# Kernel optimization log

Hardware: AMD Instinct MI355X
Metric: run time of the kernel (lower is better)

## Reference

```python
import jax, jax.numpy as jnp
import numpy as np

TAU = 2.0
V_TH = 1.0
ALPHA = 2.0  # ATan surrogate alpha (spikingjelly default)

@jax.custom_vjp
def atan_heaviside(x):
    # Forward: Heaviside spike; backward: ATan surrogate gradient.
    return (x >= 0).astype(x.dtype)

def _atan_fwd(x):
    return atan_heaviside(x), x

def _atan_bwd(x, g):
    sg = (ALPHA / 2.0) / (1.0 + (jnp.pi / 2.0 * ALPHA * x) ** 2)
    return (g * sg,)

atan_heaviside.defvjp(_atan_fwd, _atan_bwd)

def lif_scan(cur):
    # cur: [T, B, F] input currents. LIF: H = V + (X - V)/tau; S = H >= v_th; hard reset V = H*(1-S).
    def step(v, x_t):
        h = v + (x_t - v) / TAU
        s = atan_heaviside(h - V_TH)
        v_new = h * (1.0 - s)
        return v_new, s
    v0 = jnp.zeros(cur.shape[1:], dtype=cur.dtype)
    _, spikes = jax.lax.scan(step, v0, cur)
    return spikes

def setup_inputs() -> dict:
    key = jax.random.key(0)
    k1, k2 = jax.random.split(key)
    T, B, F_in, F_out = 64, 256, 1024, 1024
    x = jax.random.normal(k1, (T, B, F_in), dtype=jnp.float32)
    W = jax.random.normal(k2, (F_out, F_in), dtype=jnp.float32) * (1.0 / np.sqrt(F_in))
    return {"x": x, "W": W}

def reference(x, W):
    # Linear projection over all timesteps, then multi-step LIF recurrence.
    cur = jnp.einsum('tbf,of->tbo', x, W)  # [T, B, F_out]
    return lif_scan(cur)
```

## Files before the change

### kernel.cpp

```cpp
#include <hip/hip_runtime.h>


#define T_DIM 64
#define B_DIM 256
#define F_DIM 1024
#define K_DIM 1024
#define M_DIM 16384
#define COLS  (B_DIM * F_DIM)
#define KP    2048
#define MARGIN 6e-5f
#define LIST_CAP 32768

typedef __attribute__((ext_vector_type(8))) short short8;
typedef __attribute__((ext_vector_type(4))) float floatx4;

#define ASYNC_CP16(gp, lp)                                                     \
    __builtin_amdgcn_global_load_lds(                                          \
        (const __attribute__((address_space(1))) unsigned int*)(gp),           \
        (__attribute__((address_space(3))) unsigned int*)(lp), 16, 0, 0)

__device__ inline unsigned short f32_to_bf16_rne(float f) {
    unsigned int u = __builtin_bit_cast(unsigned int, f);
    unsigned int r = (u + 0x7FFFu + ((u >> 16) & 1u)) >> 16;
    return (unsigned short)r;
}
__device__ inline float bf16_to_f32(unsigned short h) {
    unsigned int u = ((unsigned int)h) << 16;
    return __builtin_bit_cast(float, u);
}

__global__ __launch_bounds__(256) void split_kernel(
    const float* __restrict__ x, const float* __restrict__ Wm,
    unsigned short* __restrict__ A, unsigned short* __restrict__ B,
    unsigned int* __restrict__ counter)
{
    if (blockIdx.x == 0 && threadIdx.x == 0) *counter = 0;
    const int blk = blockIdx.x;
    const float* in;
    unsigned short* dst;
    int g;
    int orow;
    if (blk < 16384) {
        g = blk * 256 + threadIdx.x;
        int e = g * 4;
        int row = e >> 10;
        orow = ((row & 255) << 6) | (row >> 8);
        in = x; dst = A;
    } else {
        g = (blk - 16384) * 256 + threadIdx.x;
        int e = g * 4;
        orow = e >> 10;
        in = Wm; dst = B;
    }
    int k = (g * 4) & 1023;
    float4 v = reinterpret_cast<const float4*>(in)[g];
    ushort4 h, l;
    float f;
    f = v.x; h.x = f32_to_bf16_rne(f); l.x = f32_to_bf16_rne(f - bf16_to_f32(h.x));
    f = v.y; h.y = f32_to_bf16_rne(f); l.y = f32_to_bf16_rne(f - bf16_to_f32(h.y));
    f = v.z; h.z = f32_to_bf16_rne(f); l.z = f32_to_bf16_rne(f - bf16_to_f32(h.z));
    f = v.w; h.w = f32_to_bf16_rne(f); l.w = f32_to_bf16_rne(f - bf16_to_f32(h.w));
    reinterpret_cast<ushort4*>(dst)[(size_t)orow * (KP / 4) + (k >> 2)] = h;
    reinterpret_cast<ushort4*>(dst)[(size_t)orow * (KP / 4) + 256 + (k >> 2)] = l;
}

__global__ __launch_bounds__(256, 2) void gemm_scan_kernel(
    const unsigned short* __restrict__ A,
    const unsigned short* __restrict__ B,
    float* __restrict__ out,
    unsigned int* __restrict__ counter, unsigned int* __restrict__ list)
{
    __shared__ unsigned short Ah[128 * 32];
    __shared__ unsigned short Al[128 * 32];
    __shared__ unsigned short Bh[256 * 32];
    __shared__ unsigned short Bl[256 * 32];

    const int tid  = threadIdx.x;
    const int lane = tid & 63;
    const int wv   = tid >> 6;
    const int lid = blockIdx.x;
    const int mt  = ((lid & 7) << 4) | (lid >> 5);
    const int nt  = (lid >> 3) & 3;
    const int m0  = mt * 128;
    const int n0  = nt * 256;
    const int wm  = (wv & 1) * 64;
    const int wn  = (wv >> 1) * 128;

    floatx4 acc[4][8] = {};

    const int srow = tid >> 2;
    const int slin = (tid & 3) * 8;
    const int ssw  = (((tid & 3) ^ ((tid >> 3) & 3)) * 8);
    const int lrow = lane & 15;
    const int q    = lane >> 4;
    const int rsw  = (lrow >> 1) & 3;

    const unsigned short* Ab = A + (size_t)m0 * KP;
    const unsigned short* Bb = B + (size_t)n0 * KP;

    for (int k0 = 0; k0 < 1024; k0 += 32) {
        __syncthreads();
        ASYNC_CP16(Ab + (size_t)srow * KP + k0 + ssw,                Ah + srow * 32 + slin);
        ASYNC_CP16(Ab + (size_t)(srow + 64) * KP + k0 + ssw,         Ah + (srow + 64) * 32 + slin);
        ASYNC_CP16(Ab + (size_t)srow * KP + 1024 + k0 + ssw,         Al + srow * 32 + slin);
        ASYNC_CP16(Ab + (size_t)(srow + 64) * KP + 1024 + k0 + ssw,  Al + (srow + 64) * 32 + slin);
        ASYNC_CP16(Bb + (size_t)srow * KP + k0 + ssw,                Bh + srow * 32 + slin);
        ASYNC_CP16(Bb + (size_t)(srow + 64) * KP + k0 + ssw,         Bh + (srow + 64) * 32 + slin);
        ASYNC_CP16(Bb + (size_t)(srow + 128) * KP + k0 + ssw,        Bh + (srow + 128) * 32 + slin);
        ASYNC_CP16(Bb + (size_t)(srow + 192) * KP + k0 + ssw,        Bh + (srow + 192) * 32 + slin);
        ASYNC_CP16(Bb + (size_t)srow * KP + 1024 + k0 + ssw,         Bl + srow * 32 + slin);
        ASYNC_CP16(Bb + (size_t)(srow + 64) * KP + 1024 + k0 + ssw,  Bl + (srow + 64) * 32 + slin);
        ASYNC_CP16(Bb + (size_t)(srow + 128) * KP + 1024 + k0 + ssw, Bl + (srow + 128) * 32 + slin);
        ASYNC_CP16(Bb + (size_t)(srow + 192) * KP + 1024 + k0 + ssw, Bl + (srow + 192) * 32 + slin);
        __syncthreads();

        const int sl = (q ^ rsw) * 8;
        short8 ah[4], al[4];
#pragma unroll
        for (int i = 0; i < 4; ++i) {
            ah[i] = *reinterpret_cast<const short8*>(&Ah[(wm + i * 16 + lrow) * 32 + sl]);
            al[i] = *reinterpret_cast<const short8*>(&Al[(wm + i * 16 + lrow) * 32 + sl]);
        }
#pragma unroll
        for (int jh = 0; jh < 2; ++jh) {
            short8 bh[4], bl[4];
#pragma unroll
            for (int j4 = 0; j4 < 4; ++j4) {
                const int jr = (wn + (jh * 4 + j4) * 16 + lrow) * 32 + sl;
                bh[j4] = *reinterpret_cast<const short8*>(&Bh[jr]);
                bl[j4] = *reinterpret_cast<const short8*>(&Bl[jr]);
            }
#pragma unroll
            for (int i = 0; i < 4; ++i)
#pragma unroll
                for (int j4 = 0; j4 < 4; ++j4)
                    acc[i][jh * 4 + j4] = __builtin_amdgcn_mfma_f32_16x16x32_bf16(
                        ah[i], bh[j4], acc[i][jh * 4 + j4], 0, 0, 0);
#pragma unroll
            for (int i = 0; i < 4; ++i)
#pragma unroll
                for (int j4 = 0; j4 < 4; ++j4)
                    acc[i][jh * 4 + j4] = __builtin_amdgcn_mfma_f32_16x16x32_bf16(
                        al[i], bh[j4], acc[i][jh * 4 + j4], 0, 0, 0);
#pragma unroll
            for (int i = 0; i < 4; ++i)
#pragma unroll
                for (int j4 = 0; j4 < 4; ++j4)
                    acc[i][jh * 4 + j4] = __builtin_amdgcn_mfma_f32_16x16x32_bf16(
                        ah[i], bl[j4], acc[i][jh * 4 + j4], 0, 0, 0);
        }
    }

    const int col = lane & 15;
    const int b_g = mt * 2 + (wv & 1);

    unsigned int fmask = 0;
#pragma unroll
    for (int j = 0; j < 8; ++j) {
        float v = 0.f;
        bool fl = false;
#pragma unroll
        for (int i = 0; i < 4; ++i) {
#pragma unroll
            for (int qq = 0; qq < 4; ++qq) {
                if (q == qq) {
#pragma unroll
                    for (int r = 0; r < 4; ++r) {
                        float cu = acc[i][j][r];
                        float h = v + (cu - v) * 0.5f;
                        float d = h - 1.0f;
                        bool sp = (d >= 0.f);
                        fl |= (fabsf(d) < MARGIN);
                        acc[i][j][r] = sp ? 1.0f : 0.0f;
                        v = sp ? 0.f : h;
                    }
                }
                v = __shfl(v, qq * 16 + col, 64);
            }
        }
        if (fl) fmask |= (1u << j);
    }
    fmask |= __shfl_xor(fmask, 16, 64);
    fmask |= __shfl_xor(fmask, 32, 64);

    float* outp = out + (size_t)b_g * F_DIM;
#pragma unroll
    for (int i = 0; i < 4; ++i)
#pragma unroll
        for (int j = 0; j < 8; ++j)
#pragma unroll
            for (int r = 0; r < 4; ++r) {
                int t = i * 16 + q * 4 + r;
                int o = n0 + wn + j * 16 + col;
                outp[(size_t)t * COLS + o] = acc[i][j][r];
            }

    if (q == 0 && fmask) {
        for (int j = 0; j < 8; ++j)
            if (fmask & (1u << j)) {
                unsigned int idx = atomicAdd(counter, 1u);
                if (idx < LIST_CAP)
                    list[idx] = (unsigned int)((b_g << 10) | (n0 + wn + j * 16 + col));
            }
    }
}

__global__ __launch_bounds__(256) void fixup_kernel(
    const float* __restrict__ x, const float* __restrict__ W,
    const unsigned int* __restrict__ counter, const unsigned int* __restrict__ list,
    float* __restrict__ out)
{
    __shared__ double curd[T_DIM];
    __shared__ float wrow[K_DIM];
    unsigned int n = *counter;
    if (n > LIST_CAP) n = LIST_CAP;
    const int wv = threadIdx.x >> 6, lane = threadIdx.x & 63;

    for (unsigned int idx = blockIdx.x; idx < n; idx += gridDim.x) {
        const unsigned int c = list[idx];
        const int b = c >> 10, o = c & 1023;
        __syncthreads();
        for (int k = threadIdx.x; k < K_DIM; k += 256) wrow[k] = W[(size_t)o * K_DIM + k];
        __syncthreads();
        for (int it = 0; it < 16; ++it) {
            const int t = it * 4 + wv;
            const float* xp = x + (size_t)t * COLS + (size_t)b * F_DIM + lane * 16;
            double s = 0.0;
#pragma unroll
            for (int qq = 0; qq < 4; ++qq) {
                float4 xv = reinterpret_cast<const float4*>(xp)[qq];
                float4 wq = *reinterpret_cast<const float4*>(&wrow[lane * 16 + qq * 4]);
                s += (double)xv.x * (double)wq.x + (double)xv.y * (double)wq.y +
                     (double)xv.z * (double)wq.z + (double)xv.w * (double)wq.w;
            }
#pragma unroll
            for (int off = 32; off > 0; off >>= 1) s += __shfl_down(s, off, 64);
            if (lane == 0) curd[t] = s;
        }
        __syncthreads();
        if (threadIdx.x == 0) {
            double v = 0.0;
            for (int t = 0; t < T_DIM; ++t) {
                double h = v + (curd[t] - v) * 0.5;
                bool s = (h >= 1.0);
                out[(size_t)t * COLS + c] = s ? 1.0f : 0.0f;
                v = s ? 0.0 : h;
            }
        }
        __syncthreads();
    }
}

#define TILE 64
#define KC 32
#define XS_LD 36
#define SC_LD 65

__global__ __launch_bounds__(256) void lif_fused_kernel(
    const float* __restrict__ x, const float* __restrict__ Wm, float* __restrict__ out)
{
    __shared__ __align__(16) unsigned char smem_raw[TILE * SC_LD * sizeof(double)];
    float* sf = reinterpret_cast<float*>(smem_raw);
    double* sd = reinterpret_cast<double*>(smem_raw);
    float* Xs = sf;
    float* Ws = sf + TILE * XS_LD;

    const int b = blockIdx.y;
    const int o0 = blockIdx.x * TILE;
    const int tid = threadIdx.x;
    const int tx = tid & 15, ty = tid >> 4;

    double acc[4][4];
#pragma unroll
    for (int i = 0; i < 4; ++i)
#pragma unroll
        for (int j = 0; j < 4; ++j) acc[i][j] = 0.0;

    const int r = tid >> 3, c4 = (tid & 7) * 4;
    const float* xbase = x + (size_t)b * F_DIM;

    for (int k0 = 0; k0 < K_DIM; k0 += KC) {
        __syncthreads();
        float4 xv0 = *reinterpret_cast<const float4*>(xbase + (size_t)r * COLS + k0 + c4);
        float4 xv1 = *reinterpret_cast<const float4*>(xbase + (size_t)(r + 32) * COLS + k0 + c4);
        *reinterpret_cast<float4*>(Xs + r * XS_LD + c4) = xv0;
        *reinterpret_cast<float4*>(Xs + (r + 32) * XS_LD + c4) = xv1;
        float4 wv0 = *reinterpret_cast<const float4*>(Wm + (size_t)(o0 + r) * K_DIM + k0 + c4);
        float4 wv1 = *reinterpret_cast<const float4*>(Wm + (size_t)(o0 + r + 32) * K_DIM + k0 + c4);
        *reinterpret_cast<float4*>(Ws + r * XS_LD + c4) = wv0;
        *reinterpret_cast<float4*>(Ws + (r + 32) * XS_LD + c4) = wv1;
        __syncthreads();
#pragma unroll 4
        for (int kk = 0; kk < KC; ++kk) {
            double xa[4], wb[4];
#pragma unroll
            for (int i = 0; i < 4; ++i) xa[i] = (double)Xs[(4 * ty + i) * XS_LD + kk];
#pragma unroll
            for (int j = 0; j < 4; ++j) wb[j] = (double)Ws[(4 * tx + j) * XS_LD + kk];
#pragma unroll
            for (int i = 0; i < 4; ++i)
#pragma unroll
                for (int j = 0; j < 4; ++j) acc[i][j] = fma(xa[i], wb[j], acc[i][j]);
        }
    }
    __syncthreads();
#pragma unroll
    for (int i = 0; i < 4; ++i)
#pragma unroll
        for (int j = 0; j < 4; ++j) sd[(4 * ty + i) * SC_LD + (4 * tx + j)] = acc[i][j];
    __syncthreads();
    if (tid < TILE) {
        double v = 0.0;
        float* outp = out + (size_t)b * F_DIM + o0 + tid;
        for (int t = 0; t < T_DIM; ++t) {
            double cu = sd[t * SC_LD + tid];
            double h = v + (cu - v) * 0.5;
            bool s = (h >= 1.0);
            outp[(size_t)t * COLS] = s ? 1.0f : 0.0f;
            v = s ? 0.0 : h;
        }
    }
}

extern "C" void kernel_launch(void* const* d_in, const int* in_sizes, int n_in,
                              void* d_out, int out_size, void* d_ws, size_t ws_size,
                              hipStream_t stream) {
    const float* x = (const float*)d_in[0];
    const float* Wm = (const float*)d_in[1];
    float* out = (float*)d_out;

    const size_t OFF_A   = 0;
    const size_t OFF_B   = OFF_A + (size_t)M_DIM * KP * 2;
    const size_t OFF_CNT = OFF_B + (size_t)F_DIM * KP * 2;
    const size_t OFF_LST = OFF_CNT + 256;
    const size_t NEEDED  = OFF_LST + (size_t)LIST_CAP * 4;

    if (ws_size < NEEDED) {
        dim3 grid(F_DIM / TILE, B_DIM, 1);
        lif_fused_kernel<<<grid, dim3(256), 0, stream>>>(x, Wm, out);
        return;
    }

    unsigned char* ws = (unsigned char*)d_ws;
    unsigned short* Abuf = (unsigned short*)(ws + OFF_A);
    unsigned short* Bbuf = (unsigned short*)(ws + OFF_B);
    unsigned int* counter = (unsigned int*)(ws + OFF_CNT);
    unsigned int* list = (unsigned int*)(ws + OFF_LST);

    split_kernel<<<dim3(16384 + 1024), dim3(256), 0, stream>>>(x, Wm, Abuf, Bbuf, counter);
    gemm_scan_kernel<<<dim3(512), dim3(256), 0, stream>>>(Abuf, Bbuf, out, counter, list);
    fixup_kernel<<<dim3(512), dim3(256), 0, stream>>>(x, Wm, counter, list, out);
}
```

Before: 225.9 us.

## Fuse fp64 fixup of near-threshold columns into GEMM-scan kernel epilogue

Removes the separate fixup kernel and its global counter and list. Each GEMM block now gathers its near-threshold columns into a shared-memory list and recomputes them itself in fp64, one wavefront per column. W is held in registers and the x load for the next timestep is prefetched. This saves a kernel launch and the global atomics, but the tail of each GEMM block gets longer and the per-block fixup work may be unbalanced. The list in shared memory reuses the Ah buffer, and its capacity is only implicitly bounded by the tile.

```diff
diff --git a/kernel.cpp b/kernel.cpp
--- a/kernel.cpp
+++ b/kernel.cpp
@@ -9,7 +9,6 @@
 #define COLS  (B_DIM * F_DIM)
 #define KP    2048
 #define MARGIN 6e-5f
-#define LIST_CAP 32768
 
 typedef __attribute__((ext_vector_type(8))) short short8;
 typedef __attribute__((ext_vector_type(4))) float floatx4;
@@ -31,10 +30,8 @@
 
 __global__ __launch_bounds__(256) void split_kernel(
     const float* __restrict__ x, const float* __restrict__ Wm,
-    unsigned short* __restrict__ A, unsigned short* __restrict__ B,
-    unsigned int* __restrict__ counter)
+    unsigned short* __restrict__ A, unsigned short* __restrict__ B)
 {
-    if (blockIdx.x == 0 && threadIdx.x == 0) *counter = 0;
     const int blk = blockIdx.x;
     const float* in;
     unsigned short* dst;
@@ -67,13 +64,15 @@
 __global__ __launch_bounds__(256, 2) void gemm_scan_kernel(
     const unsigned short* __restrict__ A,
     const unsigned short* __restrict__ B,
-    float* __restrict__ out,
-    unsigned int* __restrict__ counter, unsigned int* __restrict__ list)
+    const float* __restrict__ x,
+    const float* __restrict__ Wm,
+    float* __restrict__ out)
 {
     __shared__ unsigned short Ah[128 * 32];
     __shared__ unsigned short Al[128 * 32];
     __shared__ unsigned short Bh[256 * 32];
     __shared__ unsigned short Bl[256 * 32];
+    __shared__ unsigned int fl_cnt;
 
     const int tid  = threadIdx.x;
     const int lane = tid & 63;
@@ -195,59 +194,62 @@
                 outp[(size_t)t * COLS + o] = acc[i][j][r];
             }
 
+    unsigned int* fl_list = reinterpret_cast<unsigned int*>(Ah);
+    double* curd = reinterpret_cast<double*>(Al) + wv * 64;
+
+    __syncthreads();
+    if (tid == 0) fl_cnt = 0;
+    __syncthreads();
     if (q == 0 && fmask) {
         for (int j = 0; j < 8; ++j)
             if (fmask & (1u << j)) {
-                unsigned int idx = atomicAdd(counter, 1u);
-                if (idx < LIST_CAP)
-                    list[idx] = (unsigned int)((b_g << 10) | (n0 + wn + j * 16 + col));
-            }
-    }
-}
-
-__global__ __launch_bounds__(256) void fixup_kernel(
-    const float* __restrict__ x, const float* __restrict__ W,
-    const unsigned int* __restrict__ counter, const unsigned int* __restrict__ list,
-    float* __restrict__ out)
-{
-    __shared__ double curd[T_DIM];
-    __shared__ float wrow[K_DIM];
-    unsigned int n = *counter;
-    if (n > LIST_CAP) n = LIST_CAP;
-    const int wv = threadIdx.x >> 6, lane = threadIdx.x & 63;
-
-    for (unsigned int idx = blockIdx.x; idx < n; idx += gridDim.x) {
-        const unsigned int c = list[idx];
-        const int b = c >> 10, o = c & 1023;
-        __syncthreads();
-        for (int k = threadIdx.x; k < K_DIM; k += 256) wrow[k] = W[(size_t)o * K_DIM + k];
-        __syncthreads();
-        for (int it = 0; it < 16; ++it) {
-            const int t = it * 4 + wv;
-            const float* xp = x + (size_t)t * COLS + (size_t)b * F_DIM + lane * 16;
+                unsigned int idx = atomicAdd(&fl_cnt, 1u);
+                fl_list[idx] = (unsigned int)((b_g << 10) | (n0 + wn + j * 16 + col));
+            }
+    }
+    __syncthreads();
+    const unsigned int nfl = fl_cnt;
+
+    for (unsigned int idx = wv; idx < nfl; idx += 4) {
+        const unsigned int c = fl_list[idx];
+        const int bb = c >> 10, o = c & 1023;
+        const float* wp = Wm + (size_t)o * K_DIM + lane * 16;
+        float4 wreg[4];
+#pragma unroll
+        for (int p = 0; p < 4; ++p) wreg[p] = reinterpret_cast<const float4*>(wp)[p];
+
+        const float* xcol = x + (size_t)bb * F_DIM + lane * 16;
+        float4 xv[4];
+#pragma unroll
+        for (int p = 0; p < 4; ++p) xv[p] = reinterpret_cast<const float4*>(xcol)[p];
+
+        for (int t = 0; t < T_DIM; ++t) {
+            float4 xn[4];
+            if (t + 1 < T_DIM) {
+                const float* xp1 = xcol + (size_t)(t + 1) * COLS;
+#pragma unroll
+                for (int p = 0; p < 4; ++p) xn[p] = reinterpret_cast<const float4*>(xp1)[p];
+            }
             double s = 0.0;
 #pragma unroll
-            for (int qq = 0; qq < 4; ++qq) {
-                float4 xv = reinterpret_cast<const float4*>(xp)[qq];
-                float4 wq = *reinterpret_cast<const float4*>(&wrow[lane * 16 + qq * 4]);
-                s += (double)xv.x * (double)wq.x + (double)xv.y * (double)wq.y +
-                     (double)xv.z * (double)wq.z + (double)xv.w * (double)wq.w;
-            }
+            for (int p = 0; p < 4; ++p)
+                s += (double)xv[p].x * (double)wreg[p].x + (double)xv[p].y * (double)wreg[p].y +
+                     (double)xv[p].z * (double)wreg[p].z + (double)xv[p].w * (double)wreg[p].w;
 #pragma unroll
             for (int off = 32; off > 0; off >>= 1) s += __shfl_down(s, off, 64);
             if (lane == 0) curd[t] = s;
-        }
-        __syncthreads();
-        if (threadIdx.x == 0) {
+#pragma unroll
+            for (int p = 0; p < 4; ++p) xv[p] = xn[p];
+        }
+        if (lane == 0) {
             double v = 0.0;
             for (int t = 0; t < T_DIM; ++t) {
                 double h = v + (curd[t] - v) * 0.5;
-                bool s = (h >= 1.0);
-                out[(size_t)t * COLS + c] = s ? 1.0f : 0.0f;
-                v = s ? 0.0 : h;
-            }
-        }
-        __syncthreads();
+                bool sp = (h >= 1.0);
+                out[(size_t)t * COLS + c] = sp ? 1.0f : 0.0f;
+                v = sp ? 0.0 : h;
+            }
+        }
     }
 }
 
@@ -329,11 +331,9 @@
     const float* Wm = (const float*)d_in[1];
     float* out = (float*)d_out;
 
-    const size_t OFF_A   = 0;
-    const size_t OFF_B   = OFF_A + (size_t)M_DIM * KP * 2;
-    const size_t OFF_CNT = OFF_B + (size_t)F_DIM * KP * 2;
-    const size_t OFF_LST = OFF_CNT + 256;
-    const size_t NEEDED  = OFF_LST + (size_t)LIST_CAP * 4;
+    const size_t OFF_A  = 0;
+    const size_t OFF_B  = OFF_A + (size_t)M_DIM * KP * 2;
+    const size_t NEEDED = OFF_B + (size_t)F_DIM * KP * 2;
 
     if (ws_size < NEEDED) {
         dim3 grid(F_DIM / TILE, B_DIM, 1);
@@ -344,10 +344,7 @@
     unsigned char* ws = (unsigned char*)d_ws;
     unsigned short* Abuf = (unsigned short*)(ws + OFF_A);
     unsigned short* Bbuf = (unsigned short*)(ws + OFF_B);
-    unsigned int* counter = (unsigned int*)(ws + OFF_CNT);
-    unsigned int* list = (unsigned int*)(ws + OFF_LST);
-
-    split_kernel<<<dim3(16384 + 1024), dim3(256), 0, stream>>>(x, Wm, Abuf, Bbuf, counter);
-    gemm_scan_kernel<<<dim3(512), dim3(256), 0, stream>>>(Abuf, Bbuf, out, counter, list);
-    fixup_kernel<<<dim3(512), dim3(256), 0, stream>>>(x, Wm, counter, list, out);
-}
+
+    split_kernel<<<dim3(16384 + 1024), dim3(256), 0, stream>>>(x, Wm, Abuf, Bbuf);
+    gemm_scan_kernel<<<dim3(512), dim3(256), 0, stream>>>(Abuf, Bbuf, x, Wm, out);
+}
```

New measurement: 237.6 us. +5.2%, slower.
